# Kernel optimization log

Hardware: AMD Instinct MI355X
Metric: run time of the kernel (lower is better)

## Reference

```python
import jax, jax.numpy as jnp
import numpy as np

B, N, E, DIN, H1, H2, DOUT = 2, 20000, 320000, 128, 256, 256, 128


def setup_inputs() -> dict:
    key = jax.random.key(0)
    ks = jax.random.split(key, 9)
    X = jax.random.normal(ks[0], (B, N, DIN), dtype=jnp.float32)
    edge_index = jax.random.randint(ks[1], (2, E), 0, N, dtype=jnp.int32)
    def lin(k, fan_in, fan_out):
        lim = 1.0 / np.sqrt(fan_in)
        return jax.random.uniform(k, (fan_in, fan_out), jnp.float32, -lim, lim)
    W1 = lin(ks[2], DIN, H1); b1 = jnp.zeros((H1,), jnp.float32)
    W2 = lin(ks[3], H1, H2);  b2 = jnp.zeros((H2,), jnp.float32)
    W3 = lin(ks[4], H2, DOUT); b3 = jnp.zeros((DOUT,), jnp.float32)
    prelu_a = jnp.array(0.25, jnp.float32)  # PReLU default single shared param
    return dict(X=X, W1=W1, b1=b1, W2=W2, b2=b2, W3=W3, b3=b3,
                prelu_a=prelu_a, edge_index=edge_index)


def reference(X, W1, b1, W2, b2, W3, b3, prelu_a, edge_index):
    src, dst = edge_index[0], edge_index[1]
    n = X.shape[1]
    # GCN symmetric normalization with self-loops: deg = in-degree + 1
    deg = jax.ops.segment_sum(jnp.ones_like(src, X.dtype), dst, num_segments=n) + 1.0
    dinv = jax.lax.rsqrt(deg)                      # [N]
    norm_e = dinv[src] * dinv[dst]                 # [E] edge norm
    norm_self = dinv * dinv                        # [N] self-loop norm

    def gcn(x, W, b):
        h = x @ W                                  # [N, F_out]
        agg = jax.ops.segment_sum(h[src] * norm_e[:, None], dst, num_segments=n)
        agg = agg + h * norm_self[:, None]         # add self-loop message
        return agg + b

    def prelu(x):
        return jnp.where(x >= 0, x, prelu_a * x)

    def single(x):  # x: [N, DIN]
        x = prelu(gcn(x, W1, b1))
        x = prelu(gcn(x, W2, b2))
        return gcn(x, W3, b3)

    return jax.vmap(single)(X)                     # [B, N, DOUT]
```

## Files before the change

### kernel.cpp

```cpp
#include <hip/hip_runtime.h>

#define NB 20000
#define EB 320000
#define DIN 128
#define H1D 256
#define H2D 256
#define DOUTD 128
#define SCAN_BLOCKS ((NB + 255) / 256)

typedef __attribute__((ext_vector_type(8))) short short8;
typedef __attribute__((ext_vector_type(4))) float f32x4;

__device__ inline void bsplit(float x, unsigned short& h, unsigned short& l) {
    unsigned u = __float_as_uint(x);
    unsigned hr = (u + 0x7FFFu + ((u >> 16) & 1u)) & 0xFFFF0000u;
    h = (unsigned short)(hr >> 16);
    float lo = x - __uint_as_float(hr);
    unsigned v = __float_as_uint(lo);
    l = (unsigned short)((v + 0x7FFFu + ((v >> 16) & 1u)) >> 16);
}


__global__ void zero_kernel(int* __restrict__ p, int n) {
    int t = blockIdx.x * blockDim.x + threadIdx.x;
    if (t < n) p[t] = 0;
}

__global__ void hist_kernel(const int* __restrict__ dst, int* __restrict__ bins) {
    int t = blockIdx.x * blockDim.x + threadIdx.x;
    if (t < EB) atomicAdd(&bins[dst[t]], 1);
}

__global__ __launch_bounds__(256) void scanA_kernel(const int* __restrict__ bins,
                                                    int* __restrict__ loc,
                                                    int* __restrict__ blksum) {
    __shared__ int s[256];
    int t = threadIdx.x;
    int i = blockIdx.x * 256 + t;
    int v = (i < NB) ? bins[i] : 0;
    s[t] = v;
    __syncthreads();
    for (int off = 1; off < 256; off <<= 1) {
        int u = (t >= off) ? s[t - off] : 0;
        __syncthreads();
        s[t] += u;
        __syncthreads();
    }
    if (i < NB) loc[i] = s[t] - v;
    if (t == 255) blksum[blockIdx.x] = s[255];
}

__global__ __launch_bounds__(128) void scanB_kernel(int* __restrict__ blksum) {
    __shared__ int s[128];
    int t = threadIdx.x;
    int v = (t < SCAN_BLOCKS) ? blksum[t] : 0;
    s[t] = v;
    __syncthreads();
    for (int off = 1; off < 128; off <<= 1) {
        int u = (t >= off) ? s[t - off] : 0;
        __syncthreads();
        s[t] += u;
        __syncthreads();
    }
    if (t < SCAN_BLOCKS) blksum[t] = s[t] - v;
}

__global__ __launch_bounds__(256) void scanC_kernel(const int* __restrict__ bins,
                                                    const int* __restrict__ loc,
                                                    const int* __restrict__ blksum,
                                                    int* __restrict__ rs,
                                                    int* __restrict__ cursor,
                                                    float* __restrict__ dinv) {
    int i = blockIdx.x * 256 + threadIdx.x;
    if (i < NB) {
        int r = loc[i] + blksum[blockIdx.x];
        rs[i] = r;
        cursor[i] = r;
        dinv[i] = rsqrtf((float)bins[i] + 1.0f);
    }
    if (i == 0) rs[NB] = EB;
}

__global__ void scatter_kernel(const int* __restrict__ src, const int* __restrict__ dst,
                               const float* __restrict__ dinv,
                               int* __restrict__ cursor, int2* __restrict__ edges) {
    int t = blockIdx.x * blockDim.x + threadIdx.x;
    if (t < EB) {
        int d = dst[t], s = src[t];
        int p = atomicAdd(&cursor[d], 1);
        edges[p] = make_int2(s, __float_as_int(dinv[s] * dinv[d]));
    }
}

__global__ void wcvt_kernel(const float* __restrict__ W,
                            unsigned short* __restrict__ Wth,
                            unsigned short* __restrict__ Wtl, int K, int Nc) {
    int i = blockIdx.x * 256 + threadIdx.x;
    if (i < K * Nc) {
        int k = i / Nc, n = i % Nc;
        unsigned short h, l;
        bsplit(W[i], h, l);
        Wth[(size_t)n * K + k] = h;
        Wtl[(size_t)n * K + k] = l;
    }
}


template <int F, bool SPLIT_IN, bool SPLIT_OUT, bool BIAS, bool PRELU, int OUT>
__global__ __launch_bounds__(256) void aggv_kernel(
    const float* __restrict__ h, float* __restrict__ out,
    unsigned short* __restrict__ oh, unsigned short* __restrict__ ol,
    const int* __restrict__ rs, const int2* __restrict__ edges,
    const float* __restrict__ dinv, const float* __restrict__ bias,
    const float* __restrict__ pa, int phase) {
    const int ss = blockIdx.x & 7;
    const int chunk = blockIdx.x >> 3;
    const int wid = threadIdx.x >> 6;
    const int lane = threadIdx.x & 63;
    const int li = lane & 31;
    const int eh = lane >> 5;
    const int b = ss >> 2;
    const int c32 = (ss & 3) + phase * 4;
    const int fo = c32 * 32 + li;

    constexpr size_t GS = SPLIT_IN ? F : 2 * F;
    constexpr size_t OS = SPLIT_OUT ? F : 2 * F;
    const float* gb = h + (SPLIT_IN ? (size_t)b * NB * F : (size_t)b * F) + fo;
    float* ob = nullptr;
    unsigned short* ohb = nullptr;
    unsigned short* olb = nullptr;
    if (OUT == 0) {
        ob = out + (SPLIT_OUT ? (size_t)b * NB * F : (size_t)b * F) + fo;
    } else {
        ohb = oh + (size_t)b * F + fo;
        olb = ol + (size_t)b * F + fo;
    }

    const float pav = PRELU ? *pa : 0.0f;
    const float bval = BIAS ? bias[fo] : 0.0f;

    int n = chunk * 20 + wid * 5;
    int e1n = __builtin_amdgcn_readfirstlane(rs[n]);
    for (int j = 0; j < 5; ++j, ++n) {
        int e0 = e1n;
        e1n = __builtin_amdgcn_readfirstlane(rs[n + 1]);
        int e1 = e1n;
        float a0 = 0.f, a1 = 0.f, a2 = 0.f, a3 = 0.f;
        int e = e0;
        for (; e + 8 <= e1; e += 8) {
            int2 r0 = edges[e + eh];
            int2 r1 = edges[e + 2 + eh];
            int2 r2 = edges[e + 4 + eh];
            int2 r3 = edges[e + 6 + eh];
            float t0 = gb[(size_t)r0.x * GS];
            float t1 = gb[(size_t)r1.x * GS];
            float t2 = gb[(size_t)r2.x * GS];
            float t3 = gb[(size_t)r3.x * GS];
            a0 = fmaf(t0, __int_as_float(r0.y), a0);
            a1 = fmaf(t1, __int_as_float(r1.y), a1);
            a2 = fmaf(t2, __int_as_float(r2.y), a2);
            a3 = fmaf(t3, __int_as_float(r3.y), a3);
        }
        for (; e + 2 <= e1; e += 2) {
            int2 r0 = edges[e + eh];
            a0 = fmaf(gb[(size_t)r0.x * GS], __int_as_float(r0.y), a0);
        }
        if (e < e1) {
            int my = e + eh;
            bool valid = (my < e1);
            int2 r0 = edges[valid ? my : e];
            float w = valid ? __int_as_float(r0.y) : 0.0f;
            a0 = fmaf(gb[(size_t)r0.x * GS], w, a0);
        }
        float acc = (a0 + a1) + (a2 + a3);
        acc += __shfl_xor(acc, 32, 64);
        float dv = dinv[n];
        float r = fmaf(gb[(size_t)n * GS], dv * dv, acc);
        if (BIAS) r += bval;
        if (PRELU) r = (r >= 0.0f) ? r : pav * r;
        if (eh == 0) {
            if (OUT == 0) {
                ob[(size_t)n * OS] = r;
            } else {
                unsigned short hh, ll;
                bsplit(r, hh, ll);
                ohb[(size_t)n * 2 * F] = hh;
                olb[(size_t)n * 2 * F] = ll;
            }
        }
    }
}

template <bool BIAS, bool PRELU, int OM>
__global__ __launch_bounds__(256) void gemmb_kernel(
    const unsigned short* __restrict__ Ah, const unsigned short* __restrict__ Al, int K,
    const unsigned short* __restrict__ Wth, const unsigned short* __restrict__ Wtl, int Nc,
    const float* __restrict__ bias, const float* __restrict__ pa,
    float* __restrict__ C, unsigned short* __restrict__ Ch, unsigned short* __restrict__ Cl) {
    const int M = 2 * NB;
    __shared__ unsigned short Ash[128][40];
    __shared__ unsigned short Asl[128][40];
    __shared__ unsigned short Bsh[64][40];
    __shared__ unsigned short Bsl[64][40];

    const int t = threadIdx.x;
    const int bm = blockIdx.x * 128;
    const int bn = blockIdx.y * 64;
    const int w = t >> 6;
    const int l = t & 63;
    const int lm = l & 15;
    const int lk = (l >> 4) * 8;

    f32x4 acc[2][4];
#pragma unroll
    for (int m = 0; m < 2; ++m)
#pragma unroll
        for (int nt = 0; nt < 4; ++nt) acc[m][nt] = (f32x4){0.f, 0.f, 0.f, 0.f};

    for (int k0 = 0; k0 < K; k0 += 32) {
#pragma unroll
        for (int i = 0; i < 2; ++i) {
            int c = t + i * 256;
            int row = c >> 2, seg = (c & 3) * 8;
            int gr = bm + row;
            short8 vh = (short8){0, 0, 0, 0, 0, 0, 0, 0};
            short8 vl = vh;
            if (gr < M) {
                vh = *(const short8*)&Ah[(size_t)gr * K + k0 + seg];
                vl = *(const short8*)&Al[(size_t)gr * K + k0 + seg];
            }
            *(short8*)&Ash[row][seg] = vh;
            *(short8*)&Asl[row][seg] = vl;
        }
        {
            int n = t >> 2, seg = (t & 3) * 8;
            *(short8*)&Bsh[n][seg] = *(const short8*)&Wth[(size_t)(bn + n) * K + k0 + seg];
            *(short8*)&Bsl[n][seg] = *(const short8*)&Wtl[(size_t)(bn + n) * K + k0 + seg];
        }
        __syncthreads();

        short8 ah0 = *(const short8*)&Ash[w * 32 + lm][lk];
        short8 ah1 = *(const short8*)&Ash[w * 32 + 16 + lm][lk];
        short8 al0 = *(const short8*)&Asl[w * 32 + lm][lk];
        short8 al1 = *(const short8*)&Asl[w * 32 + 16 + lm][lk];
#pragma unroll
        for (int nt = 0; nt < 4; ++nt) {
            short8 bh = *(const short8*)&Bsh[nt * 16 + lm][lk];
            short8 bl = *(const short8*)&Bsl[nt * 16 + lm][lk];
            acc[0][nt] = __builtin_amdgcn_mfma_f32_16x16x32_bf16(ah0, bh, acc[0][nt], 0, 0, 0);
            acc[0][nt] = __builtin_amdgcn_mfma_f32_16x16x32_bf16(ah0, bl, acc[0][nt], 0, 0, 0);
            acc[0][nt] = __builtin_amdgcn_mfma_f32_16x16x32_bf16(al0, bh, acc[0][nt], 0, 0, 0);
            acc[1][nt] = __builtin_amdgcn_mfma_f32_16x16x32_bf16(ah1, bh, acc[1][nt], 0, 0, 0);
            acc[1][nt] = __builtin_amdgcn_mfma_f32_16x16x32_bf16(ah1, bl, acc[1][nt], 0, 0, 0);
            acc[1][nt] = __builtin_amdgcn_mfma_f32_16x16x32_bf16(al1, bh, acc[1][nt], 0, 0, 0);
        }
        __syncthreads();
    }

    const float pav = PRELU ? *pa : 0.0f;
    const int lg = l >> 4;
#pragma unroll
    for (int m = 0; m < 2; ++m) {
#pragma unroll
        for (int nt = 0; nt < 4; ++nt) {
            int col = bn + nt * 16 + lm;
            float bv = BIAS ? bias[col] : 0.0f;
#pragma unroll
            for (int j = 0; j < 4; ++j) {
                int row = bm + w * 32 + m * 16 + lg * 4 + j;
                if (row < M) {
                    float r = acc[m][nt][j] + bv;
                    if (PRELU) r = (r >= 0.0f) ? r : pav * r;
                    if (OM == 0) {
                        C[(size_t)row * Nc + col] = r;
                    } else {
                        unsigned short hh, ll;
                        bsplit(r, hh, ll);
                        Ch[(size_t)row * Nc + col] = hh;
                        Cl[(size_t)row * Nc + col] = ll;
                    }
                }
            }
        }
    }
}


static inline char* carve(char*& p, size_t bytes) {
    char* r = p;
    p += (bytes + 255) & ~(size_t)255;
    return r;
}

extern "C" void kernel_launch(void* const* d_in, const int* in_sizes, int n_in,
                              void* d_out, int out_size, void* d_ws, size_t ws_size,
                              hipStream_t stream) {
    const float* X  = (const float*)d_in[0];
    const float* W1 = (const float*)d_in[1];
    const float* b1 = (const float*)d_in[2];
    const float* W2 = (const float*)d_in[3];
    const float* b2 = (const float*)d_in[4];
    const float* W3 = (const float*)d_in[5];
    const float* b3 = (const float*)d_in[6];
    const float* pa = (const float*)d_in[7];
    const int* ei   = (const int*)d_in[8];
    const int* src = ei;
    const int* dst = ei + EB;
    float* out = (float*)d_out;

    char* p = (char*)d_ws;
    int* bins    = (int*)carve(p, NB * sizeof(int));
    int* loc     = (int*)carve(p, NB * sizeof(int));
    int* blksum  = (int*)carve(p, 128 * sizeof(int));
    int* rs      = (int*)carve(p, (NB + 1) * sizeof(int));
    int* cursor  = (int*)carve(p, NB * sizeof(int));
    int2* edges  = (int2*)carve(p, EB * sizeof(int2));
    float* dinv  = (float*)carve(p, NB * sizeof(float));
    unsigned short* W1th = (unsigned short*)carve(p, DIN * H1D * 2);
    unsigned short* W1tl = (unsigned short*)carve(p, DIN * H1D * 2);
    unsigned short* W2th = (unsigned short*)carve(p, H1D * H2D * 2);
    unsigned short* W2tl = (unsigned short*)carve(p, H1D * H2D * 2);
    unsigned short* W3th = (unsigned short*)carve(p, H2D * DOUTD * 2);
    unsigned short* W3tl = (unsigned short*)carve(p, H2D * DOUTD * 2);
    char* U = carve(p, (size_t)2 * NB * 256 * sizeof(float));
    char* V = carve(p, (size_t)2 * NB * 256 * sizeof(float));

    const int M = 2 * NB;
    unsigned short* A1h = (unsigned short*)U;
    unsigned short* A1l = A1h + (size_t)M * DIN;
    float* R = (float*)U;
    float* T = (float*)U;
    unsigned short* G1h = (unsigned short*)V;
    unsigned short* G1l = G1h + (size_t)M * H1D;
    unsigned short* Sh = (unsigned short*)V;
    unsigned short* Sl = Sh + (size_t)M * H2D;

    zero_kernel<<<SCAN_BLOCKS, 256, 0, stream>>>(bins, NB);
    hist_kernel<<<(EB + 255) / 256, 256, 0, stream>>>(dst, bins);
    scanA_kernel<<<SCAN_BLOCKS, 256, 0, stream>>>(bins, loc, blksum);
    scanB_kernel<<<1, 128, 0, stream>>>(blksum);
    scanC_kernel<<<SCAN_BLOCKS, 256, 0, stream>>>(bins, loc, blksum, rs, cursor, dinv);
    scatter_kernel<<<(EB + 255) / 256, 256, 0, stream>>>(src, dst, dinv, cursor, edges);
    wcvt_kernel<<<(DIN * H1D + 255) / 256, 256, 0, stream>>>(W1, W1th, W1tl, DIN, H1D);
    wcvt_kernel<<<(H1D * H2D + 255) / 256, 256, 0, stream>>>(W2, W2th, W2tl, H1D, H2D);
    wcvt_kernel<<<(H2D * DOUTD + 255) / 256, 256, 0, stream>>>(W3, W3th, W3tl, H2D, DOUTD);

    const int AGGV = 8000;
    const int MT2 = (M + 127) / 128;

    aggv_kernel<128, true, false, false, false, 1><<<AGGV, 256, 0, stream>>>(
        X, nullptr, A1h, A1l, rs, edges, dinv, nullptr, nullptr, 0);

    gemmb_kernel<true, true, 1><<<dim3(MT2, H1D / 64), 256, 0, stream>>>(
        A1h, A1l, DIN, W1th, W1tl, H1D, b1, pa, nullptr, G1h, G1l);

    gemmb_kernel<false, false, 0><<<dim3(MT2, H2D / 64), 256, 0, stream>>>(
        G1h, G1l, H1D, W2th, W2tl, H2D, nullptr, nullptr, R, nullptr, nullptr);

    aggv_kernel<256, false, false, true, true, 1><<<AGGV, 256, 0, stream>>>(
        R, nullptr, Sh, Sl, rs, edges, dinv, b2, pa, 0);
    aggv_kernel<256, false, false, true, true, 1><<<AGGV, 256, 0, stream>>>(
        R, nullptr, Sh, Sl, rs, edges, dinv, b2, pa, 1);

    gemmb_kernel<false, false, 0><<<dim3(MT2, DOUTD / 64), 256, 0, stream>>>(
        Sh, Sl, H2D, W3th, W3tl, DOUTD, nullptr, nullptr, T, nullptr, nullptr);

    aggv_kernel<128, false, true, true, false, 0><<<AGGV, 256, 0, stream>>>(
        T, out, nullptr, nullptr, rs, edges, dinv, b3, nullptr, 0);
}
```

Baseline: 442.1 us.

## Pipeline the two batch items across fused GEMM and aggregation launches

Splits the batch into two independent per-sample streams and staggers them. Each launch pairs the GEMM of one sample with the sparse aggregation of the other inside a single grid, so compute-bound MFMA work overlaps memory-bound gathers. The GEMMs now read fp32 activations and split them to bf16 hi/lo in-kernel instead of materializing split buffers. Per-sample contiguous layouts replace the interleaved batch layout. This adds branchy mixed-role kernels with different shared memory and register needs, which may reduce occupancy, and uses the output buffer as scratch.

```diff
diff --git a/kernel.cpp b/kernel.cpp
--- a/kernel.cpp
+++ b/kernel.cpp
@@ -6,7 +6,9 @@
 #define H1D 256
 #define H2D 256
 #define DOUTD 128
-#define SCAN_BLOCKS ((NB + 255) / 256)
+#define SCAN_BLOCKS 79
+#define MT64 313
+#define MT128 157
 
 typedef __attribute__((ext_vector_type(8))) short short8;
 typedef __attribute__((ext_vector_type(4))) float f32x4;
@@ -18,6 +20,20 @@
     float lo = x - __uint_as_float(hr);
     unsigned v = __float_as_uint(lo);
     l = (unsigned short)((v + 0x7FFFu + ((v >> 16) & 1u)) >> 16);
+}
+
+__device__ inline void cvt4(float4 v, unsigned& h01, unsigned& h23,
+                            unsigned& l01, unsigned& l23) {
+    unsigned u0 = __float_as_uint(v.x), u1 = __float_as_uint(v.y);
+    unsigned u2 = __float_as_uint(v.z), u3 = __float_as_uint(v.w);
+    h01 = (u0 >> 16) | (u1 & 0xFFFF0000u);
+    h23 = (u2 >> 16) | (u3 & 0xFFFF0000u);
+    float f0 = v.x - __uint_as_float(u0 & 0xFFFF0000u);
+    float f1 = v.y - __uint_as_float(u1 & 0xFFFF0000u);
+    float f2 = v.z - __uint_as_float(u2 & 0xFFFF0000u);
+    float f3 = v.w - __uint_as_float(u3 & 0xFFFF0000u);
+    l01 = (__float_as_uint(f0) >> 16) | (__float_as_uint(f1) & 0xFFFF0000u);
+    l23 = (__float_as_uint(f2) >> 16) | (__float_as_uint(f3) & 0xFFFF0000u);
 }
 
 
@@ -106,40 +122,29 @@
 }
 
 
-template <int F, bool SPLIT_IN, bool SPLIT_OUT, bool BIAS, bool PRELU, int OUT>
-__global__ __launch_bounds__(256) void aggv_kernel(
-    const float* __restrict__ h, float* __restrict__ out,
-    unsigned short* __restrict__ oh, unsigned short* __restrict__ ol,
-    const int* __restrict__ rs, const int2* __restrict__ edges,
-    const float* __restrict__ dinv, const float* __restrict__ bias,
-    const float* __restrict__ pa, int phase) {
-    const int ss = blockIdx.x & 7;
-    const int chunk = blockIdx.x >> 3;
+template <int F, bool BIAS, bool PRELU>
+__device__ void aggv_body(int a, int ss,
+                          const float* __restrict__ h, float* __restrict__ out,
+                          const int* __restrict__ rs, const int2* __restrict__ edges,
+                          const float* __restrict__ dinv, const float* __restrict__ bias,
+                          const float* __restrict__ pa) {
+    constexpr int NS = F / 32;
+    constexpr int NH = 8 / NS;
+    const int half = (NH == 2) ? (ss >> 2) : 0;
+    const int c32 = ss & (NS - 1);
+    const int chunk = a >> 3;
     const int wid = threadIdx.x >> 6;
     const int lane = threadIdx.x & 63;
     const int li = lane & 31;
     const int eh = lane >> 5;
-    const int b = ss >> 2;
-    const int c32 = (ss & 3) + phase * 4;
     const int fo = c32 * 32 + li;
 
-    constexpr size_t GS = SPLIT_IN ? F : 2 * F;
-    constexpr size_t OS = SPLIT_OUT ? F : 2 * F;
-    const float* gb = h + (SPLIT_IN ? (size_t)b * NB * F : (size_t)b * F) + fo;
-    float* ob = nullptr;
-    unsigned short* ohb = nullptr;
-    unsigned short* olb = nullptr;
-    if (OUT == 0) {
-        ob = out + (SPLIT_OUT ? (size_t)b * NB * F : (size_t)b * F) + fo;
-    } else {
-        ohb = oh + (size_t)b * F + fo;
-        olb = ol + (size_t)b * F + fo;
-    }
-
+    const float* gb = h + fo;
+    float* ob = out + fo;
     const float pav = PRELU ? *pa : 0.0f;
     const float bval = BIAS ? bias[fo] : 0.0f;
 
-    int n = chunk * 20 + wid * 5;
+    int n = half * (NB / NH) + chunk * 20 + wid * 5;
     int e1n = __builtin_amdgcn_readfirstlane(rs[n]);
     for (int j = 0; j < 5; ++j, ++n) {
         int e0 = e1n;
@@ -152,10 +157,10 @@
             int2 r1 = edges[e + 2 + eh];
             int2 r2 = edges[e + 4 + eh];
             int2 r3 = edges[e + 6 + eh];
-            float t0 = gb[(size_t)r0.x * GS];
-            float t1 = gb[(size_t)r1.x * GS];
-            float t2 = gb[(size_t)r2.x * GS];
-            float t3 = gb[(size_t)r3.x * GS];
+            float t0 = gb[(size_t)r0.x * F];
+            float t1 = gb[(size_t)r1.x * F];
+            float t2 = gb[(size_t)r2.x * F];
+            float t3 = gb[(size_t)r3.x * F];
             a0 = fmaf(t0, __int_as_float(r0.y), a0);
             a1 = fmaf(t1, __int_as_float(r1.y), a1);
             a2 = fmaf(t2, __int_as_float(r2.y), a2);
@@ -163,53 +168,111 @@
         }
         for (; e + 2 <= e1; e += 2) {
             int2 r0 = edges[e + eh];
-            a0 = fmaf(gb[(size_t)r0.x * GS], __int_as_float(r0.y), a0);
+            a0 = fmaf(gb[(size_t)r0.x * F], __int_as_float(r0.y), a0);
         }
         if (e < e1) {
             int my = e + eh;
             bool valid = (my < e1);
             int2 r0 = edges[valid ? my : e];
             float w = valid ? __int_as_float(r0.y) : 0.0f;
-            a0 = fmaf(gb[(size_t)r0.x * GS], w, a0);
+            a0 = fmaf(gb[(size_t)r0.x * F], w, a0);
         }
         float acc = (a0 + a1) + (a2 + a3);
         acc += __shfl_xor(acc, 32, 64);
         float dv = dinv[n];
-        float r = fmaf(gb[(size_t)n * GS], dv * dv, acc);
+        float r = fmaf(gb[(size_t)n * F], dv * dv, acc);
         if (BIAS) r += bval;
         if (PRELU) r = (r >= 0.0f) ? r : pav * r;
-        if (eh == 0) {
-            if (OUT == 0) {
-                ob[(size_t)n * OS] = r;
-            } else {
-                unsigned short hh, ll;
-                bsplit(r, hh, ll);
-                ohb[(size_t)n * 2 * F] = hh;
-                olb[(size_t)n * 2 * F] = ll;
+        if (eh == 0) ob[(size_t)n * F] = r;
+    }
+}
+
+
+template <bool BIAS, bool PRELU>
+__device__ void gemm64_body(char* smem, int gx, const float* __restrict__ A, int K,
+                            const unsigned short* __restrict__ Wth,
+                            const unsigned short* __restrict__ Wtl, int Nc,
+                            const float* __restrict__ bias, const float* __restrict__ pa,
+                            float* __restrict__ C) {
+    const int M = NB;
+    unsigned short (*Ash)[40] = (unsigned short(*)[40])smem;
+    unsigned short (*Asl)[40] = (unsigned short(*)[40])(smem + 5120);
+    unsigned short (*Bsh)[40] = (unsigned short(*)[40])(smem + 10240);
+    unsigned short (*Bsl)[40] = (unsigned short(*)[40])(smem + 15360);
+    const int t = threadIdx.x;
+    const int bm = (gx % MT64) * 64;
+    const int bn = (gx / MT64) * 64;
+    const int w = t >> 6, l = t & 63, lm = l & 15, lg = l >> 4;
+    const int lk = lg * 8;
+    const int sr = t >> 2, sc = (t & 3) * 8;
+
+    f32x4 acc[4];
+#pragma unroll
+    for (int nt = 0; nt < 4; ++nt) acc[nt] = (f32x4){0.f, 0.f, 0.f, 0.f};
+
+    for (int k0 = 0; k0 < K; k0 += 32) {
+        float4 va = make_float4(0.f, 0.f, 0.f, 0.f), vb = va;
+        int gr = bm + sr;
+        if (gr < M) {
+            va = *(const float4*)&A[(size_t)gr * K + k0 + sc];
+            vb = *(const float4*)&A[(size_t)gr * K + k0 + sc + 4];
+        }
+        unsigned h01, h23, l01, l23, h45, h67, l45, l67;
+        cvt4(va, h01, h23, l01, l23);
+        cvt4(vb, h45, h67, l45, l67);
+        *(uint4*)&Ash[sr][sc] = make_uint4(h01, h23, h45, h67);
+        *(uint4*)&Asl[sr][sc] = make_uint4(l01, l23, l45, l67);
+        *(short8*)&Bsh[sr][sc] = *(const short8*)&Wth[(size_t)(bn + sr) * K + k0 + sc];
+        *(short8*)&Bsl[sr][sc] = *(const short8*)&Wtl[(size_t)(bn + sr) * K + k0 + sc];
+        __syncthreads();
+        short8 ah = *(const short8*)&Ash[w * 16 + lm][lk];
+        short8 al = *(const short8*)&Asl[w * 16 + lm][lk];
+#pragma unroll
+        for (int nt = 0; nt < 4; ++nt) {
+            short8 bh = *(const short8*)&Bsh[nt * 16 + lm][lk];
+            short8 bl = *(const short8*)&Bsl[nt * 16 + lm][lk];
+            acc[nt] = __builtin_amdgcn_mfma_f32_16x16x32_bf16(ah, bh, acc[nt], 0, 0, 0);
+            acc[nt] = __builtin_amdgcn_mfma_f32_16x16x32_bf16(ah, bl, acc[nt], 0, 0, 0);
+            acc[nt] = __builtin_amdgcn_mfma_f32_16x16x32_bf16(al, bh, acc[nt], 0, 0, 0);
+        }
+        __syncthreads();
+    }
+
+    const float pav = PRELU ? *pa : 0.0f;
+#pragma unroll
+    for (int nt = 0; nt < 4; ++nt) {
+        int col = bn + nt * 16 + lm;
+        float bv = BIAS ? bias[col] : 0.0f;
+#pragma unroll
+        for (int j = 0; j < 4; ++j) {
+            int row = bm + w * 16 + lg * 4 + j;
+            if (row < M) {
+                float r = acc[nt][j] + bv;
+                if (PRELU) r = (r >= 0.0f) ? r : pav * r;
+                __builtin_nontemporal_store(r, &C[(size_t)row * Nc + col]);
             }
         }
     }
 }
 
-template <bool BIAS, bool PRELU, int OM>
-__global__ __launch_bounds__(256) void gemmb_kernel(
-    const unsigned short* __restrict__ Ah, const unsigned short* __restrict__ Al, int K,
-    const unsigned short* __restrict__ Wth, const unsigned short* __restrict__ Wtl, int Nc,
-    const float* __restrict__ bias, const float* __restrict__ pa,
-    float* __restrict__ C, unsigned short* __restrict__ Ch, unsigned short* __restrict__ Cl) {
-    const int M = 2 * NB;
-    __shared__ unsigned short Ash[128][40];
-    __shared__ unsigned short Asl[128][40];
-    __shared__ unsigned short Bsh[64][40];
-    __shared__ unsigned short Bsl[64][40];
-
+template <bool BIAS, bool PRELU>
+__device__ void gemm128_body(char* smem, int gx, const float* __restrict__ A, int K,
+                             const unsigned short* __restrict__ Wth,
+                             const unsigned short* __restrict__ Wtl, int Nc,
+                             const float* __restrict__ bias, const float* __restrict__ pa,
+                             float* __restrict__ C) {
+    const int M = NB;
+    unsigned short (*Ash)[40] = (unsigned short(*)[40])smem;
+    unsigned short (*Asl)[40] = (unsigned short(*)[40])(smem + 10240);
+    unsigned short (*Bsh)[40] = (unsigned short(*)[40])(smem + 20480);
+    unsigned short (*Bsl)[40] = (unsigned short(*)[40])(smem + 25600);
     const int t = threadIdx.x;
-    const int bm = blockIdx.x * 128;
-    const int bn = blockIdx.y * 64;
-    const int w = t >> 6;
-    const int l = t & 63;
-    const int lm = l & 15;
-    const int lk = (l >> 4) * 8;
+    const int bm = (gx % MT128) * 128;
+    const int bn = (gx / MT128) * 64;
+    const int w = t >> 6, l = t & 63, lm = l & 15, lg = l >> 4;
+    const int lk = lg * 8;
+    const int ar = t >> 1, ac = (t & 1) * 16;
+    const int br = t >> 2, bc = (t & 3) * 8;
 
     f32x4 acc[2][4];
 #pragma unroll
@@ -218,27 +281,24 @@
         for (int nt = 0; nt < 4; ++nt) acc[m][nt] = (f32x4){0.f, 0.f, 0.f, 0.f};
 
     for (int k0 = 0; k0 < K; k0 += 32) {
-#pragma unroll
-        for (int i = 0; i < 2; ++i) {
-            int c = t + i * 256;
-            int row = c >> 2, seg = (c & 3) * 8;
-            int gr = bm + row;
-            short8 vh = (short8){0, 0, 0, 0, 0, 0, 0, 0};
-            short8 vl = vh;
+        int gr = bm + ar;
+#pragma unroll
+        for (int hseg = 0; hseg < 2; ++hseg) {
+            int cc = ac + hseg * 8;
+            float4 va = make_float4(0.f, 0.f, 0.f, 0.f), vb = va;
             if (gr < M) {
-                vh = *(const short8*)&Ah[(size_t)gr * K + k0 + seg];
-                vl = *(const short8*)&Al[(size_t)gr * K + k0 + seg];
+                va = *(const float4*)&A[(size_t)gr * K + k0 + cc];
+                vb = *(const float4*)&A[(size_t)gr * K + k0 + cc + 4];
             }
-            *(short8*)&Ash[row][seg] = vh;
-            *(short8*)&Asl[row][seg] = vl;
-        }
-        {
-            int n = t >> 2, seg = (t & 3) * 8;
-            *(short8*)&Bsh[n][seg] = *(const short8*)&Wth[(size_t)(bn + n) * K + k0 + seg];
-            *(short8*)&Bsl[n][seg] = *(const short8*)&Wtl[(size_t)(bn + n) * K + k0 + seg];
-        }
-        __syncthreads();
-
+            unsigned h01, h23, l01, l23, h45, h67, l45, l67;
+            cvt4(va, h01, h23, l01, l23);
+            cvt4(vb, h45, h67, l45, l67);
+            *(uint4*)&Ash[ar][cc] = make_uint4(h01, h23, h45, h67);
+            *(uint4*)&Asl[ar][cc] = make_uint4(l01, l23, l45, l67);
+        }
+        *(short8*)&Bsh[br][bc] = *(const short8*)&Wth[(size_t)(bn + br) * K + k0 + bc];
+        *(short8*)&Bsl[br][bc] = *(const short8*)&Wtl[(size_t)(bn + br) * K + k0 + bc];
+        __syncthreads();
         short8 ah0 = *(const short8*)&Ash[w * 32 + lm][lk];
         short8 ah1 = *(const short8*)&Ash[w * 32 + 16 + lm][lk];
         short8 al0 = *(const short8*)&Asl[w * 32 + lm][lk];
@@ -258,7 +318,6 @@
     }
 
     const float pav = PRELU ? *pa : 0.0f;
-    const int lg = l >> 4;
 #pragma unroll
     for (int m = 0; m < 2; ++m) {
 #pragma unroll
@@ -271,18 +330,55 @@
                 if (row < M) {
                     float r = acc[m][nt][j] + bv;
                     if (PRELU) r = (r >= 0.0f) ? r : pav * r;
-                    if (OM == 0) {
-                        C[(size_t)row * Nc + col] = r;
-                    } else {
-                        unsigned short hh, ll;
-                        bsplit(r, hh, ll);
-                        Ch[(size_t)row * Nc + col] = hh;
-                        Cl[(size_t)row * Nc + col] = ll;
-                    }
+                    C[(size_t)row * Nc + col] = r;
                 }
             }
         }
     }
+}
+
+
+template <int F, bool BIAS, bool PRELU>
+__global__ __launch_bounds__(256) void aggv_kernel(
+    const float* __restrict__ h, float* __restrict__ out,
+    const int* __restrict__ rs, const int2* __restrict__ edges,
+    const float* __restrict__ dinv, const float* __restrict__ bias,
+    const float* __restrict__ pa) {
+    aggv_body<F, BIAS, PRELU>(blockIdx.x, blockIdx.x & 7, h, out, rs, edges,
+                              dinv, bias, pa);
+}
+
+template <int AF, bool AB, bool AP, bool GB_, bool GP>
+__global__ __launch_bounds__(256) void fat64_kernel(
+    const float* __restrict__ A, int K,
+    const unsigned short* __restrict__ Wth, const unsigned short* __restrict__ Wtl,
+    int Nc, const float* __restrict__ gbias, float* __restrict__ C, int ng,
+    const float* __restrict__ ah, float* __restrict__ aout,
+    const int* __restrict__ rs, const int2* __restrict__ edges,
+    const float* __restrict__ dinv, const float* __restrict__ abias,
+    const float* __restrict__ pa) {
+    __shared__ char smem[20480];
+    int bx = blockIdx.x;
+    if (bx < ng) {
+        gemm64_body<GB_, GP>(smem, bx, A, K, Wth, Wtl, Nc, gbias, pa, C);
+    } else {
+        aggv_body<AF, AB, AP>(bx - ng, bx & 7, ah, aout, rs, edges, dinv, abias, pa);
+    }
+}
+
+template <bool B1, bool P1, bool B2, bool P2>
+__global__ __launch_bounds__(256) void gemm2_kernel(
+    const float* __restrict__ A1p, int K1,
+    const unsigned short* __restrict__ W1h, const unsigned short* __restrict__ W1l,
+    int N1, const float* __restrict__ bias1, float* __restrict__ C1, int ng1,
+    const float* __restrict__ A2p, int K2,
+    const unsigned short* __restrict__ W2h, const unsigned short* __restrict__ W2l,
+    int N2, const float* __restrict__ bias2, float* __restrict__ C2,
+    const float* __restrict__ pa) {
+    __shared__ char smem[30720];
+    int bx = blockIdx.x;
+    if (bx < ng1) gemm128_body<B1, P1>(smem, bx, A1p, K1, W1h, W1l, N1, bias1, pa, C1);
+    else          gemm128_body<B2, P2>(smem, bx - ng1, A2p, K2, W2h, W2l, N2, bias2, pa, C2);
 }
 
 
@@ -322,18 +418,19 @@
     unsigned short* W2tl = (unsigned short*)carve(p, H1D * H2D * 2);
     unsigned short* W3th = (unsigned short*)carve(p, H2D * DOUTD * 2);
     unsigned short* W3tl = (unsigned short*)carve(p, H2D * DOUTD * 2);
-    char* U = carve(p, (size_t)2 * NB * 256 * sizeof(float));
-    char* V = carve(p, (size_t)2 * NB * 256 * sizeof(float));
-
-    const int M = 2 * NB;
-    unsigned short* A1h = (unsigned short*)U;
-    unsigned short* A1l = A1h + (size_t)M * DIN;
-    float* R = (float*)U;
-    float* T = (float*)U;
-    unsigned short* G1h = (unsigned short*)V;
-    unsigned short* G1l = G1h + (size_t)M * H1D;
-    unsigned short* Sh = (unsigned short*)V;
-    unsigned short* Sl = Sh + (size_t)M * H2D;
+    float* P0 = (float*)carve(p, (size_t)NB * DIN * sizeof(float));
+    float* P1 = (float*)carve(p, (size_t)NB * DIN * sizeof(float));
+    float* Q0 = (float*)carve(p, (size_t)NB * H1D * sizeof(float));
+    float* Q1 = (float*)carve(p, (size_t)NB * H1D * sizeof(float));
+    float* R1 = (float*)carve(p, (size_t)NB * H2D * sizeof(float));
+    float* R0 = (float*)d_out;
+    float* S0 = Q0; float* S1 = Q1;
+    float* T0 = P0; float* T1 = P1;
+
+    const float* X0 = X;
+    const float* X1 = X + (size_t)NB * DIN;
+    float* out0 = out;
+    float* out1 = out + (size_t)NB * DOUTD;
 
     zero_kernel<<<SCAN_BLOCKS, 256, 0, stream>>>(bins, NB);
     hist_kernel<<<(EB + 255) / 256, 256, 0, stream>>>(dst, bins);
@@ -345,26 +442,38 @@
     wcvt_kernel<<<(H1D * H2D + 255) / 256, 256, 0, stream>>>(W2, W2th, W2tl, H1D, H2D);
     wcvt_kernel<<<(H2D * DOUTD + 255) / 256, 256, 0, stream>>>(W3, W3th, W3tl, H2D, DOUTD);
 
-    const int AGGV = 8000;
-    const int MT2 = (M + 127) / 128;
-
-    aggv_kernel<128, true, false, false, false, 1><<<AGGV, 256, 0, stream>>>(
-        X, nullptr, A1h, A1l, rs, edges, dinv, nullptr, nullptr, 0);
-
-    gemmb_kernel<true, true, 1><<<dim3(MT2, H1D / 64), 256, 0, stream>>>(
-        A1h, A1l, DIN, W1th, W1tl, H1D, b1, pa, nullptr, G1h, G1l);
-
-    gemmb_kernel<false, false, 0><<<dim3(MT2, H2D / 64), 256, 0, stream>>>(
-        G1h, G1l, H1D, W2th, W2tl, H2D, nullptr, nullptr, R, nullptr, nullptr);
-
-    aggv_kernel<256, false, false, true, true, 1><<<AGGV, 256, 0, stream>>>(
-        R, nullptr, Sh, Sl, rs, edges, dinv, b2, pa, 0);
-    aggv_kernel<256, false, false, true, true, 1><<<AGGV, 256, 0, stream>>>(
-        R, nullptr, Sh, Sl, rs, edges, dinv, b2, pa, 1);
-
-    gemmb_kernel<false, false, 0><<<dim3(MT2, DOUTD / 64), 256, 0, stream>>>(
-        Sh, Sl, H2D, W3th, W3tl, DOUTD, nullptr, nullptr, T, nullptr, nullptr);
-
-    aggv_kernel<128, false, true, true, false, 0><<<AGGV, 256, 0, stream>>>(
-        T, out, nullptr, nullptr, rs, edges, dinv, b3, nullptr, 0);
-}
+    const int NA128 = 4000;
+    const int NA256 = 8000;
+    const int NG1_64 = MT64 * (H1D / 64);
+    const int NG2_64 = MT64 * (H2D / 64);
+    const int NG3_64 = MT64 * (DOUTD / 64);
+    const int NG2_128 = MT128 * (H2D / 64);
+    const int NG1_128 = MT128 * (H1D / 64);
+
+
+    aggv_kernel<128, false, false><<<NA128, 256, 0, stream>>>(
+        X0, P0, rs, edges, dinv, nullptr, nullptr);
+
+    fat64_kernel<128, false, false, true, true><<<NG1_64 + NA128, 256, 0, stream>>>(
+        P0, DIN, W1th, W1tl, H1D, b1, Q0, NG1_64,
+        X1, P1, rs, edges, dinv, nullptr, pa);
+
+    gemm2_kernel<false, false, true, true><<<NG2_128 + NG1_128, 256, 0, stream>>>(
+        Q0, H1D, W2th, W2tl, H2D, nullptr, R0, NG2_128,
+        P1, DIN, W1th, W1tl, H1D, b1, Q1, pa);
+
+    fat64_kernel<256, true, true, false, false><<<NG2_64 + NA256, 256, 0, stream>>>(
+        Q1, H1D, W2th, W2tl, H2D, nullptr, R1, NG2_64,
+        R0, S0, rs, edges, dinv, b2, pa);
+
+    fat64_kernel<256, true, true, false, false><<<NG3_64 + NA256, 256, 0, stream>>>(
+        S0, H2D, W3th, W3tl, DOUTD, nullptr, T0, NG3_64,
+        R1, S1, rs, edges, dinv, b2, pa);
+
+    fat64_kernel<128, true, false, false, false><<<NG3_64 + NA128, 256, 0, stream>>>(
+        S1, H2D, W3th, W3tl, DOUTD, nullptr, T1, NG3_64,
+        T0, out0, rs, edges, dinv, b3, pa);
+
+    aggv_kernel<128, true, false><<<NA128, 256, 0, stream>>>(
+        T1, out1, rs, edges, dinv, b3, nullptr);
+}
```

New measurement: 418.6 us. 5.3% less time.
